# Kernel tuning notes

Measured on AMD Instinct MI355X. Metric: run time of the kernel, lower is better.

The kernel has to match this reference:

```python
import jax, jax.numpy as jnp
import numpy as np

K = 7          # kernel_size (window)
PAD = (K - 1) // 2  # SAME padding for stride 1


def setup_inputs() -> dict:
    key = jax.random.key(0)
    ks = jax.random.split(key, 7)
    B, H, W, C, F = 8, 128, 128, 256, 256
    rs = F // 2  # rel_size
    return {
        "x": jax.random.normal(ks[0], (B, H, W, C), jnp.float32),
        "Wq": jax.random.normal(ks[1], (C, F), jnp.float32) * 0.05,
        "Wk": jax.random.normal(ks[2], (C, F), jnp.float32) * 0.05,
        "Wv": jax.random.normal(ks[3], (C, F), jnp.float32) * 0.05,
        "rel_x": jax.random.normal(ks[4], (rs, K), jnp.float32) * 0.05,
        "rel_y": jax.random.normal(ks[5], (F - rs, K), jnp.float32) * 0.05,
        "bias": jax.random.normal(ks[6], (1, 1, 1, F), jnp.float32) * (1.0 / np.sqrt(F).astype(np.float32)),
    }


def reference(x, Wq, Wk, Wv, rel_x, rel_y, bias):
    B, H, W, C = x.shape
    rs = rel_x.shape[0]
    # 1x1 conv projections (single group)
    q = jnp.einsum('bhwc,cf->bhwf', x, Wq)
    k = jnp.einsum('bhwc,cf->bhwf', x, Wk)
    v = jnp.einsum('bhwc,cf->bhwf', x, Wv)
    kp = jnp.pad(k, ((0, 0), (PAD, PAD), (PAD, PAD), (0, 0)))
    vp = jnp.pad(v, ((0, 0), (PAD, PAD), (PAD, PAD), (0, 0)))
    # window scores: sum_c q * shifted(k) -> [b,h,w,kh,kw]; avoids im2col blowup
    scores = jnp.stack([
        jnp.stack([jnp.einsum('bhwf,bhwf->bhw', q, kp[:, i:i + H, j:j + W, :])
                   for j in range(K)], axis=-1)
        for i in range(K)], axis=-2)
    # relative position terms: x-half broadcasts along rows (kh), y-half along cols (kw)
    qx = jnp.einsum('bhwx,xk->bhwk', q[..., :rs], rel_x)
    qy = jnp.einsum('bhwy,yk->bhwk', q[..., rs:], rel_y)
    scores = scores + qx[:, :, :, None, :] + qy[:, :, :, :, None]
    attn = jax.nn.softmax(scores.reshape(B, H, W, K * K), axis=-1).reshape(B, H, W, K, K)
    # attention-weighted sum over the window for each channel
    out = sum(attn[:, :, :, i, j][..., None] * vp[:, i:i + H, j:j + W, :]
              for i in range(K) for j in range(K))
    return out + bias
```

## Files before the change

### kernel.cpp

```cpp
#include <hip/hip_runtime.h>
#include <hip/hip_fp16.h>
#include <stdint.h>

typedef _Float16 half8 __attribute__((ext_vector_type(8)));
typedef _Float16 half2v __attribute__((ext_vector_type(2)));
typedef __attribute__((ext_vector_type(4))) float f32x4;

__device__ __forceinline__ unsigned short f2h(float f) {
  __half h = __float2half(f);
  unsigned short u; __builtin_memcpy(&u, &h, 2); return u;
}
__device__ __forceinline__ unsigned pk2h(float a, float b) {
  auto v = __builtin_amdgcn_cvt_pkrtz(a, b);
  unsigned u; __builtin_memcpy(&u, &v, 4); return u;
}
__device__ __forceinline__ half2v h2cast(unsigned u) {
  half2v v; __builtin_memcpy(&v, &u, 4); return v;
}

#if __has_builtin(__builtin_amdgcn_fdot2)
__device__ __forceinline__ float dot2(half2v a, half2v b, float c) {
  return __builtin_amdgcn_fdot2(a, b, c, false);
}
#else
__device__ __forceinline__ float dot2(half2v a, half2v b, float c) {
  return c + (float)a[0] * (float)b[0] + (float)a[1] * (float)b[1];
}
#endif

__device__ __forceinline__ void gl_lds16(const void* g, void* l) {
  __builtin_amdgcn_global_load_lds(
      (const __attribute__((address_space(1))) void*)g,
      (__attribute__((address_space(3))) void*)l, 16, 0, 0);
}

__global__ __launch_bounds__(256) void prep(const float* __restrict__ x,
                                            const float* __restrict__ Wq,
                                            const float* __restrict__ Wk,
                                            const float* __restrict__ Wv,
                                            unsigned short* __restrict__ xh,
                                            unsigned short* __restrict__ Wb) {
  const int bid = blockIdx.x;
  if (bid < 16384) {
    const size_t i = ((size_t)bid * 256 + threadIdx.x) * 8;
    float4 a = *(const float4*)&x[i];
    float4 b = *(const float4*)&x[i + 4];
    uint4 o;
    o.x = pk2h(a.x, a.y); o.y = pk2h(a.z, a.w);
    o.z = pk2h(b.x, b.y); o.w = pk2h(b.z, b.w);
    *(uint4*)&xh[i] = o;
  } else {
    const int e = bid - 16384;
    const int w = e >> 8;
    const int n = e & 255;
    const float* W = (w == 0) ? Wq : ((w == 1) ? Wk : Wv);
    const int k = threadIdx.x;
    Wb[(size_t)e * 256 + k] = f2h(W[(size_t)k * 256 + n]);
  }
}

__global__ __launch_bounds__(256) void qkv_gemm(const unsigned short* __restrict__ xh,
                                                const unsigned short* __restrict__ Wb,
                                                unsigned short* __restrict__ qkv) {
  __shared__ unsigned char ldsb[32768];

  const int tid = threadIdx.x;
  const int l = tid & 63, l15 = l & 15, l4 = l >> 4;
  const int wv = tid >> 6, wr = wv >> 1, wc = wv & 1;

  const int pid = blockIdx.x;
  const int cid = (pid & 7) * 768 + (pid >> 3);
  const int by = cid / 6;
  const int bx = cid - by * 6;
  const size_t row0 = (size_t)by * 128;
  const int n0 = bx * 128;

  const int rbase0 = wv * 32, rbase1 = wv * 32 + 16;
  const int rA0 = rbase0 + (l >> 2), rA1 = rbase1 + (l >> 2);
  const int q0 = (l & 3) ^ ((rA0 >> 1) & 3), q1 = (l & 3) ^ ((rA1 >> 1) & 3);
  const unsigned short* gA0 = xh + (row0 + rA0) * 256 + q0 * 8;
  const unsigned short* gA1 = xh + (row0 + rA1) * 256 + q1 * 8;
  const unsigned short* gB0 = Wb + (size_t)(n0 + rA0) * 256 + q0 * 8;
  const unsigned short* gB1 = Wb + (size_t)(n0 + rA1) * 256 + q1 * 8;

  f32x4 acc[4][4] = {};

  auto stage = [&](int s, int d) {
    gl_lds16(gA0 + s * 32, &ldsb[d * 8192 + rbase0 * 64]);
    gl_lds16(gA1 + s * 32, &ldsb[d * 8192 + rbase1 * 64]);
    gl_lds16(gB0 + s * 32, &ldsb[16384 + d * 8192 + rbase0 * 64]);
    gl_lds16(gB1 + s * 32, &ldsb[16384 + d * 8192 + rbase1 * 64]);
  };

  stage(0, 0);
  __syncthreads();

  for (int s = 0; s < 8; ++s) {
    const int d = s & 1;
    if (s < 7) stage(s + 1, d ^ 1);
    half8 af[4], bf[4];
#pragma unroll
    for (int m = 0; m < 4; ++m) {
      const int r = wr * 64 + m * 16 + l15;
      af[m] = *(const half8*)&ldsb[d * 8192 + r * 64 + ((l4 ^ ((r >> 1) & 3)) * 16)];
    }
#pragma unroll
    for (int n = 0; n < 4; ++n) {
      const int r = wc * 64 + n * 16 + l15;
      bf[n] = *(const half8*)&ldsb[16384 + d * 8192 + r * 64 + ((l4 ^ ((r >> 1) & 3)) * 16)];
    }
#pragma unroll
    for (int n = 0; n < 4; ++n)
#pragma unroll
      for (int m = 0; m < 4; ++m)
        acc[m][n] = __builtin_amdgcn_mfma_f32_16x16x32_f16(af[m], bf[n], acc[m][n], 0, 0, 0);
    __syncthreads();
  }

#pragma unroll
  for (int m = 0; m < 4; ++m)
#pragma unroll
    for (int n = 0; n < 4; ++n) {
      const int ng = n0 + wc * 64 + n * 16 + l15;
      unsigned short* op = qkv + (size_t)(ng >> 8) * 33554432 + (ng & 255);
#pragma unroll
      for (int r = 0; r < 4; ++r) {
        const size_t grow = row0 + wr * 64 + m * 16 + l4 * 4 + r;
        op[grow * 256] = f2h(acc[m][n][r]);
      }
    }
}

__global__ __launch_bounds__(256) void qrel(const unsigned short* __restrict__ q,
                                            const float* __restrict__ relx,
                                            const float* __restrict__ rely,
                                            unsigned short* __restrict__ qr) {
  __shared__ unsigned wpk[896];
  for (int i = threadIdx.x; i < 896; i += 256) {
    const int hf = (i >= 448) ? 1 : 0;
    const int r = i - hf * 448;
    const int c2 = r / 7, j = r - c2 * 7;
    const float* R = hf ? rely : relx;
    wpk[i] = pk2h(R[(2 * c2) * 7 + j], R[(2 * c2 + 1) * 7 + j]);
  }
  __syncthreads();
  const size_t pix = (size_t)blockIdx.x * 256 + threadIdx.x;
  const uint4* qp = (const uint4*)(q + pix * 256);
  float ax[7] = {0, 0, 0, 0, 0, 0, 0}, ay[7] = {0, 0, 0, 0, 0, 0, 0};
#pragma unroll
  for (int g = 0; g < 32; ++g) {
    const uint4 u = qp[g];
    const int c2b = (g & 15) * 4;
    if (g < 16) {
#pragma unroll
      for (int j = 0; j < 7; ++j) {
        float s = ax[j];
        s = dot2(h2cast(u.x), h2cast(wpk[(c2b + 0) * 7 + j]), s);
        s = dot2(h2cast(u.y), h2cast(wpk[(c2b + 1) * 7 + j]), s);
        s = dot2(h2cast(u.z), h2cast(wpk[(c2b + 2) * 7 + j]), s);
        s = dot2(h2cast(u.w), h2cast(wpk[(c2b + 3) * 7 + j]), s);
        ax[j] = s;
      }
    } else {
#pragma unroll
      for (int j = 0; j < 7; ++j) {
        float s = ay[j];
        s = dot2(h2cast(u.x), h2cast(wpk[448 + (c2b + 0) * 7 + j]), s);
        s = dot2(h2cast(u.y), h2cast(wpk[448 + (c2b + 1) * 7 + j]), s);
        s = dot2(h2cast(u.z), h2cast(wpk[448 + (c2b + 2) * 7 + j]), s);
        s = dot2(h2cast(u.w), h2cast(wpk[448 + (c2b + 3) * 7 + j]), s);
        ay[j] = s;
      }
    }
  }
  uint4 o0, o1;
  o0.x = pk2h(ax[0], ax[1]); o0.y = pk2h(ax[2], ax[3]);
  o0.z = pk2h(ax[4], ax[5]); o0.w = pk2h(ax[6], ay[0]);
  o1.x = pk2h(ay[1], ay[2]); o1.y = pk2h(ay[3], ay[4]);
  o1.z = pk2h(ay[5], ay[6]); o1.w = 0;
  uint4* dst = (uint4*)(qr + pix * 512);
  dst[0] = o0; dst[1] = o1;
}

__global__ __launch_bounds__(512, 2) void attn(const unsigned short* __restrict__ qkv,
                                               const float* __restrict__ bias,
                                               const unsigned short* __restrict__ qrelb,
                                               float* __restrict__ out) {
  __shared__ unsigned short kv[2][4][4256];

  const int tid = threadIdx.x;
  const int wv = tid >> 6;
  const int lo = tid & 15, hi = (tid >> 4) & 3;
  const int rp = wv >> 1;
  const int ch16 = (wv & 1) * 16;

  const int q = tid >> 7;
  const int pa = (tid >> 5) & 3;
  const int pc = tid & 31;

  const int pid = blockIdx.x;
  const int cid = (pid & 7) * 64 + (pid >> 3);
  const int ht = cid & 15, wt = (cid >> 4) & 3, b = cid >> 6;

  const int hA = ht * 8 + 2 * pa, wA = wt * 32 + pc;
  const size_t pixA = (size_t)((b * 128 + hA) * 128 + wA);
  const size_t pixB = pixA + 128;
  const int pxA = 2 * pa * 32 + pc;
  const int pxB = pxA + 32;

  const unsigned short* qb = qkv;
  const unsigned short* kb = qkv + 33554432;
  const unsigned short* vb = qkv + 67108864;

  const int pr0 = tid / 38, pc0 = tid - pr0 * 38;
  const int gh0 = ht * 8 + pr0 - 3, gw0 = wt * 32 + pc0 - 3;
  const bool ok0 = ((unsigned)gh0 < 128u) && ((unsigned)gw0 < 128u);
  const long long go0 = ((long long)((b * 128 + gh0) * 128 + gw0)) * 256;

  const int p1 = tid + 512;
  const int pr1 = p1 / 38, pc1 = p1 - pr1 * 38;
  const int gh1 = ht * 8 + pr1 - 3, gw1 = wt * 32 + pc1 - 3;
  const bool ok1 = (p1 < 532) && ((unsigned)gh1 < 128u) && ((unsigned)gw1 < 128u);
  const long long go1 = ((long long)((b * 128 + gh1) * 128 + gw1)) * 256;

  auto stage = [&](const unsigned short* base, int c, int d) {
#pragma unroll
    for (int g = 0; g < 4; ++g) {
      if (ok0) gl_lds16(base + go0 + c * 32 + g * 8, &kv[d][g][wv * 512]);
      if (ok1) gl_lds16(base + go1 + c * 32 + g * 8, &kv[d][g][4096]);
    }
  };

  auto zero_oob = [&]() {
    const uint4 z = make_uint4(0u, 0u, 0u, 0u);
    for (int p = tid; p < 532; p += 512) {
      const int pr = p / 38, pcx = p - pr * 38;
      const int gh = ht * 8 + pr - 3, gw = wt * 32 + pcx - 3;
      if (!((unsigned)gh < 128u && (unsigned)gw < 128u)) {
#pragma unroll
        for (int d = 0; d < 2; ++d)
#pragma unroll
          for (int g = 0; g < 4; ++g)
            *(uint4*)&kv[d][g][p * 8] = z;
      }
    }
  };

  zero_oob();
  stage(kb, 0, 0);
  __syncthreads();

  int slot0[7];
#pragma unroll
  for (int t = 0; t < 7; ++t) {
    const int p = t * 16 + lo;
    const int ur = p / 14, uc = p - ur * 14;
    slot0[t] = (2 * rp + ur) * 38 + ch16 + uc;
  }
  const size_t qpix =
      (size_t)((b * 128 + ht * 8 + 2 * rp + (lo >> 3)) * 128 + wt * 32 + ch16 + (lo & 7));
  const unsigned short* qlane = qb + qpix * 256 + hi * 8;

  f32x4 acc[2][7] = {};

  for (int s = 0; s < 8; ++s) {
    const int d = s & 1;
    if (s < 7) stage(kb, s + 1, d ^ 1);
    half8 qf[2];
#pragma unroll
    for (int g = 0; g < 2; ++g)
      qf[g] = *(const half8*)(qlane + (size_t)g * 2048 + s * 32);
    const unsigned short* kpl = &kv[d][hi][0];
    __builtin_amdgcn_s_setprio(1);
    half8 kf[7][2];
#pragma unroll
    for (int t = 0; t < 7; ++t) {
      const unsigned short* kt = kpl + slot0[t] * 8;
      kf[t][0] = *(const half8*)(kt);
      kf[t][1] = *(const half8*)(kt + 64);
    }
#pragma unroll
    for (int t = 0; t < 7; ++t) {
      acc[0][t] = __builtin_amdgcn_mfma_f32_16x16x32_f16(qf[0], kf[t][0], acc[0][t], 0, 0, 0);
      acc[1][t] = __builtin_amdgcn_mfma_f32_16x16x32_f16(qf[1], kf[t][1], acc[1][t], 0, 0, 0);
    }
    __builtin_amdgcn_s_setprio(0);
    __syncthreads();
  }

  float* pbuf = (float*)&kv[0][0][0];
#pragma unroll
  for (int t = 0; t < 7; ++t) {
    const int p = t * 16 + lo;
    const int ur = p / 14, uc = p - ur * 14;
#pragma unroll
    for (int r = 0; r < 4; ++r) {
      const int qq = hi * 4 + r;
      const int di = ur - (qq >> 3), dj = uc - (qq & 7);
      if (((unsigned)di < 7u) && ((unsigned)dj < 7u)) {
        const int pslot = di * 7 + dj;
#pragma unroll
        for (int g = 0; g < 2; ++g) {
          const int prow_ = (2 * rp + (qq >> 3)) * 32 + ch16 + 8 * g + (qq & 7);
          pbuf[prow_ * 52 + pslot] = acc[g][t][r];
        }
      }
    }
  }
  __syncthreads();

  unsigned pwp[49];
  {
    float sc[49];
    const float* prow = pbuf + pxA * 52;
#pragma unroll
    for (int k = 0; k < 12; ++k) {
      const float4 v = ((const float4*)prow)[k];
      sc[k * 4 + 0] = v.x; sc[k * 4 + 1] = v.y;
      sc[k * 4 + 2] = v.z; sc[k * 4 + 3] = v.w;
    }
    sc[48] = prow[48];
    const uint4* rpq = (const uint4*)(qrelb + pixA * 512);
    uint4 r0 = rpq[0], r1 = rpq[1];
    half2v a0 = h2cast(r0.x), a1 = h2cast(r0.y), a2 = h2cast(r0.z), a3 = h2cast(r0.w);
    half2v b0 = h2cast(r1.x), b1 = h2cast(r1.y), b2 = h2cast(r1.z);
    float qx[7] = {a0[0], a0[1], a1[0], a1[1], a2[0], a2[1], a3[0]};
    float qy[7] = {a3[1], b0[0], b0[1], b1[0], b1[1], b2[0], b2[1]};
#pragma unroll
    for (int i = 0; i < 7; ++i)
#pragma unroll
      for (int j = 0; j < 7; ++j) sc[i * 7 + j] += qx[j] + qy[i];
    float mx = sc[0];
#pragma unroll
    for (int t = 1; t < 49; ++t) mx = fmaxf(mx, sc[t]);
    float sum = 0.0f;
#pragma unroll
    for (int t = 0; t < 49; ++t) {
      float e = __expf(sc[t] - mx);
      sc[t] = e;
      sum += e;
    }
    const float invs = 1.0f / sum;
#pragma unroll
    for (int t = 0; t < 49; ++t) pwp[t] = (unsigned)f2h(sc[t] * invs);
  }
  {
    float sc[49];
    const float* prow = pbuf + pxB * 52;
#pragma unroll
    for (int k = 0; k < 12; ++k) {
      const float4 v = ((const float4*)prow)[k];
      sc[k * 4 + 0] = v.x; sc[k * 4 + 1] = v.y;
      sc[k * 4 + 2] = v.z; sc[k * 4 + 3] = v.w;
    }
    sc[48] = prow[48];
    const uint4* rpq = (const uint4*)(qrelb + pixB * 512);
    uint4 r0 = rpq[0], r1 = rpq[1];
    half2v a0 = h2cast(r0.x), a1 = h2cast(r0.y), a2 = h2cast(r0.z), a3 = h2cast(r0.w);
    half2v b0 = h2cast(r1.x), b1 = h2cast(r1.y), b2 = h2cast(r1.z);
    float qx[7] = {a0[0], a0[1], a1[0], a1[1], a2[0], a2[1], a3[0]};
    float qy[7] = {a3[1], b0[0], b0[1], b1[0], b1[1], b2[0], b2[1]};
#pragma unroll
    for (int i = 0; i < 7; ++i)
#pragma unroll
      for (int j = 0; j < 7; ++j) sc[i * 7 + j] += qx[j] + qy[i];
    float mx = sc[0];
#pragma unroll
    for (int t = 1; t < 49; ++t) mx = fmaxf(mx, sc[t]);
    float sum = 0.0f;
#pragma unroll
    for (int t = 0; t < 49; ++t) {
      float e = __expf(sc[t] - mx);
      sc[t] = e;
      sum += e;
    }
    const float invs = 1.0f / sum;
#pragma unroll
    for (int t = 0; t < 49; ++t) pwp[t] |= ((unsigned)f2h(sc[t] * invs)) << 16;
  }
  __syncthreads();

  zero_oob();
  stage(vb, 0, 0);
  __syncthreads();

  for (int s = 0; s < 8; ++s) {
    const int d = s & 1;
    const int f0 = s * 32 + q * 8;
    if (s < 7) stage(vb, s + 1, d ^ 1);
    half2v accA[4], accB[4];
#pragma unroll
    for (int a2 = 0; a2 < 4; ++a2) {
      accA[a2] = half2v{(_Float16)0, (_Float16)0};
      accB[a2] = half2v{(_Float16)0, (_Float16)0};
    }
    __builtin_amdgcn_s_setprio(1);
#pragma unroll
    for (int ub = 0; ub < 4; ++ub) {
      const int u0 = 2 * ub, u1 = u0 + 1;
      const int r0b = ((2 * pa + u0) * 38 + pc) * 8;
      const int r1b = ((2 * pa + u1) * 38 + pc) * 8;
      uint4 ua[14];
#pragma unroll
      for (int j = 0; j < 7; ++j) {
        ua[j] = *(const uint4*)&kv[d][q][r0b + j * 8];
        ua[7 + j] = *(const uint4*)&kv[d][q][r1b + j * 8];
      }
#pragma unroll
      for (int j = 0; j < 7; ++j) {
        {
          const half2v pp = h2cast(pwp[u0 * 7 + j]);
          const half2v p2 = half2v{pp[0], pp[0]};
          accA[0] += p2 * h2cast(ua[j].x);
          accA[1] += p2 * h2cast(ua[j].y);
          accA[2] += p2 * h2cast(ua[j].z);
          accA[3] += p2 * h2cast(ua[j].w);
        }
        if (ub > 0) {
          const half2v pp = h2cast(pwp[(u0 - 1) * 7 + j]);
          const half2v p2 = half2v{pp[1], pp[1]};
          accB[0] += p2 * h2cast(ua[j].x);
          accB[1] += p2 * h2cast(ua[j].y);
          accB[2] += p2 * h2cast(ua[j].z);
          accB[3] += p2 * h2cast(ua[j].w);
        }
      }
#pragma unroll
      for (int j = 0; j < 7; ++j) {
        if (ub < 3) {
          const half2v pp = h2cast(pwp[u1 * 7 + j]);
          const half2v p2 = half2v{pp[0], pp[0]};
          accA[0] += p2 * h2cast(ua[7 + j].x);
          accA[1] += p2 * h2cast(ua[7 + j].y);
          accA[2] += p2 * h2cast(ua[7 + j].z);
          accA[3] += p2 * h2cast(ua[7 + j].w);
        }
        {
          const half2v pp = h2cast(pwp[(u1 - 1) * 7 + j]);
          const half2v p2 = half2v{pp[1], pp[1]};
          accB[0] += p2 * h2cast(ua[7 + j].x);
          accB[1] += p2 * h2cast(ua[7 + j].y);
          accB[2] += p2 * h2cast(ua[7 + j].z);
          accB[3] += p2 * h2cast(ua[7 + j].w);
        }
      }
    }
    __builtin_amdgcn_s_setprio(0);
#pragma unroll
    for (int fq = 0; fq < 2; ++fq) {
      float4 bv = *(const float4*)&bias[f0 + fq * 4];
      float4 oA, oB;
      oA.x = (float)accA[fq * 2 + 0][0] + bv.x;
      oA.y = (float)accA[fq * 2 + 0][1] + bv.y;
      oA.z = (float)accA[fq * 2 + 1][0] + bv.z;
      oA.w = (float)accA[fq * 2 + 1][1] + bv.w;
      oB.x = (float)accB[fq * 2 + 0][0] + bv.x;
      oB.y = (float)accB[fq * 2 + 0][1] + bv.y;
      oB.z = (float)accB[fq * 2 + 1][0] + bv.z;
      oB.w = (float)accB[fq * 2 + 1][1] + bv.w;
      *(float4*)&out[pixA * 256 + f0 + fq * 4] = oA;
      *(float4*)&out[pixB * 256 + f0 + fq * 4] = oB;
    }
    if (s < 7) __syncthreads();
  }
}

extern "C" void kernel_launch(void* const* d_in, const int* in_sizes, int n_in,
                              void* d_out, int out_size, void* d_ws, size_t ws_size,
                              hipStream_t stream) {
  const float* x = (const float*)d_in[0];
  const float* Wq = (const float*)d_in[1];
  const float* Wk = (const float*)d_in[2];
  const float* Wv = (const float*)d_in[3];
  const float* relx = (const float*)d_in[4];
  const float* rely = (const float*)d_in[5];
  const float* bias = (const float*)d_in[6];
  float* out = (float*)d_out;

  unsigned short* xh = (unsigned short*)d_out;
  unsigned short* qrl = (unsigned short*)d_out;
  unsigned short* Wb = (unsigned short*)d_ws;
  unsigned short* qkv = (unsigned short*)((char*)d_ws + 393216);

  prep<<<dim3(17152), dim3(256), 0, stream>>>(x, Wq, Wk, Wv, xh, Wb);
  qkv_gemm<<<dim3(6144), dim3(256), 0, stream>>>(xh, Wb, qkv);
  qrel<<<dim3(512), dim3(256), 0, stream>>>(qkv, relx, rely, qrl);
  attn<<<dim3(512), dim3(512), 0, stream>>>(qkv, bias, qrl, out);
}
```

Measured before the change: 273.7 us.

## Fuse relative-position projection into attention kernel using already-loaded q fragments

Removes the separate qrel kernel and computes the q·rel_x / q·rel_y terms inside the attention kernel. It reuses the q fragments already loaded for the score MFMAs, does dot2 accumulation per stage, reduces across lanes with shuffles, and stores packed results in LDS for the softmax. This drops a kernel launch and a global round-trip of the q tensor plus the qrel buffer. In exchange it adds LDS usage, extra VALU work and register pressure in the main loop, which could lower occupancy.

```diff
diff --git a/kernel.cpp b/kernel.cpp
--- a/kernel.cpp
+++ b/kernel.cpp
@@ -131,62 +131,14 @@
     }
 }
 
-__global__ __launch_bounds__(256) void qrel(const unsigned short* __restrict__ q,
-                                            const float* __restrict__ relx,
-                                            const float* __restrict__ rely,
-                                            unsigned short* __restrict__ qr) {
-  __shared__ unsigned wpk[896];
-  for (int i = threadIdx.x; i < 896; i += 256) {
-    const int hf = (i >= 448) ? 1 : 0;
-    const int r = i - hf * 448;
-    const int c2 = r / 7, j = r - c2 * 7;
-    const float* R = hf ? rely : relx;
-    wpk[i] = pk2h(R[(2 * c2) * 7 + j], R[(2 * c2 + 1) * 7 + j]);
-  }
-  __syncthreads();
-  const size_t pix = (size_t)blockIdx.x * 256 + threadIdx.x;
-  const uint4* qp = (const uint4*)(q + pix * 256);
-  float ax[7] = {0, 0, 0, 0, 0, 0, 0}, ay[7] = {0, 0, 0, 0, 0, 0, 0};
-#pragma unroll
-  for (int g = 0; g < 32; ++g) {
-    const uint4 u = qp[g];
-    const int c2b = (g & 15) * 4;
-    if (g < 16) {
-#pragma unroll
-      for (int j = 0; j < 7; ++j) {
-        float s = ax[j];
-        s = dot2(h2cast(u.x), h2cast(wpk[(c2b + 0) * 7 + j]), s);
-        s = dot2(h2cast(u.y), h2cast(wpk[(c2b + 1) * 7 + j]), s);
-        s = dot2(h2cast(u.z), h2cast(wpk[(c2b + 2) * 7 + j]), s);
-        s = dot2(h2cast(u.w), h2cast(wpk[(c2b + 3) * 7 + j]), s);
-        ax[j] = s;
-      }
-    } else {
-#pragma unroll
-      for (int j = 0; j < 7; ++j) {
-        float s = ay[j];
-        s = dot2(h2cast(u.x), h2cast(wpk[448 + (c2b + 0) * 7 + j]), s);
-        s = dot2(h2cast(u.y), h2cast(wpk[448 + (c2b + 1) * 7 + j]), s);
-        s = dot2(h2cast(u.z), h2cast(wpk[448 + (c2b + 2) * 7 + j]), s);
-        s = dot2(h2cast(u.w), h2cast(wpk[448 + (c2b + 3) * 7 + j]), s);
-        ay[j] = s;
-      }
-    }
-  }
-  uint4 o0, o1;
-  o0.x = pk2h(ax[0], ax[1]); o0.y = pk2h(ax[2], ax[3]);
-  o0.z = pk2h(ax[4], ax[5]); o0.w = pk2h(ax[6], ay[0]);
-  o1.x = pk2h(ay[1], ay[2]); o1.y = pk2h(ay[3], ay[4]);
-  o1.z = pk2h(ay[5], ay[6]); o1.w = 0;
-  uint4* dst = (uint4*)(qr + pix * 512);
-  dst[0] = o0; dst[1] = o1;
-}
-
 __global__ __launch_bounds__(512, 2) void attn(const unsigned short* __restrict__ qkv,
                                                const float* __restrict__ bias,
-                                               const unsigned short* __restrict__ qrelb,
+                                               const float* __restrict__ relx,
+                                               const float* __restrict__ rely,
                                                float* __restrict__ out) {
   __shared__ unsigned short kv[2][4][4256];
+  __shared__ unsigned wpk[896];
+  __shared__ unsigned qrl_lds[256 * 7];
 
   const int tid = threadIdx.x;
   const int wv = tid >> 6;
@@ -246,6 +198,14 @@
     }
   };
 
+  for (int i = tid; i < 896; i += 512) {
+    const int hf = (i >= 448) ? 1 : 0;
+    const int r = i - hf * 448;
+    const int c2 = r / 7, j = r - c2 * 7;
+    const float* R = hf ? rely : relx;
+    wpk[i] = pk2h(R[(2 * c2) * 7 + j], R[(2 * c2 + 1) * 7 + j]);
+  }
+
   zero_oob();
   stage(kb, 0, 0);
   __syncthreads();
@@ -262,6 +222,7 @@
   const unsigned short* qlane = qb + qpix * 256 + hi * 8;
 
   f32x4 acc[2][7] = {};
+  float qxp[2][7] = {}, qyp[2][7] = {};
 
   for (int s = 0; s < 8; ++s) {
     const int d = s & 1;
@@ -285,7 +246,66 @@
       acc[1][t] = __builtin_amdgcn_mfma_f32_16x16x32_f16(qf[1], kf[t][1], acc[1][t], 0, 0, 0);
     }
     __builtin_amdgcn_s_setprio(0);
+    if (s < 4) {
+      const int cb = s * 16 + hi * 4;
+#pragma unroll
+      for (int g = 0; g < 2; ++g) {
+        uint4 qw; __builtin_memcpy(&qw, &qf[g], 16);
+#pragma unroll
+        for (int j = 0; j < 7; ++j) {
+          float v = qxp[g][j];
+          v = dot2(h2cast(qw.x), h2cast(wpk[(cb + 0) * 7 + j]), v);
+          v = dot2(h2cast(qw.y), h2cast(wpk[(cb + 1) * 7 + j]), v);
+          v = dot2(h2cast(qw.z), h2cast(wpk[(cb + 2) * 7 + j]), v);
+          v = dot2(h2cast(qw.w), h2cast(wpk[(cb + 3) * 7 + j]), v);
+          qxp[g][j] = v;
+        }
+      }
+    } else {
+      const int cb = (s - 4) * 16 + hi * 4;
+#pragma unroll
+      for (int g = 0; g < 2; ++g) {
+        uint4 qw; __builtin_memcpy(&qw, &qf[g], 16);
+#pragma unroll
+        for (int j = 0; j < 7; ++j) {
+          float v = qyp[g][j];
+          v = dot2(h2cast(qw.x), h2cast(wpk[448 + (cb + 0) * 7 + j]), v);
+          v = dot2(h2cast(qw.y), h2cast(wpk[448 + (cb + 1) * 7 + j]), v);
+          v = dot2(h2cast(qw.z), h2cast(wpk[448 + (cb + 2) * 7 + j]), v);
+          v = dot2(h2cast(qw.w), h2cast(wpk[448 + (cb + 3) * 7 + j]), v);
+          qyp[g][j] = v;
+        }
+      }
+    }
     __syncthreads();
+  }
+
+#pragma unroll
+  for (int g = 0; g < 2; ++g)
+#pragma unroll
+    for (int j = 0; j < 7; ++j) {
+      float vx = qxp[g][j];
+      vx += __shfl_xor(vx, 16, 64);
+      vx += __shfl_xor(vx, 32, 64);
+      qxp[g][j] = vx;
+      float vy = qyp[g][j];
+      vy += __shfl_xor(vy, 16, 64);
+      vy += __shfl_xor(vy, 32, 64);
+      qyp[g][j] = vy;
+    }
+  if (hi == 0) {
+#pragma unroll
+    for (int g = 0; g < 2; ++g) {
+      const int prow_ = (2 * rp + (lo >> 3)) * 32 + ch16 + 8 * g + (lo & 7);
+      unsigned* dst = &qrl_lds[prow_ * 7];
+      dst[0] = pk2h(qxp[g][0], qxp[g][1]);
+      dst[1] = pk2h(qxp[g][2], qxp[g][3]);
+      dst[2] = pk2h(qxp[g][4], qxp[g][5]);
+      dst[3] = pk2h(qxp[g][6], qyp[g][0]);
+      dst[4] = pk2h(qyp[g][1], qyp[g][2]);
+      dst[5] = pk2h(qyp[g][3], qyp[g][4]);
+      dst[6] = pk2h(qyp[g][5], qyp[g][6]);
+    }
   }
 
   float* pbuf = (float*)&kv[0][0][0];
@@ -320,10 +340,9 @@
       sc[k * 4 + 2] = v.z; sc[k * 4 + 3] = v.w;
     }
     sc[48] = prow[48];
-    const uint4* rpq = (const uint4*)(qrelb + pixA * 512);
-    uint4 r0 = rpq[0], r1 = rpq[1];
-    half2v a0 = h2cast(r0.x), a1 = h2cast(r0.y), a2 = h2cast(r0.z), a3 = h2cast(r0.w);
-    half2v b0 = h2cast(r1.x), b1 = h2cast(r1.y), b2 = h2cast(r1.z);
+    const unsigned* qr = &qrl_lds[pxA * 7];
+    half2v a0 = h2cast(qr[0]), a1 = h2cast(qr[1]), a2 = h2cast(qr[2]), a3 = h2cast(qr[3]);
+    half2v b0 = h2cast(qr[4]), b1 = h2cast(qr[5]), b2 = h2cast(qr[6]);
     float qx[7] = {a0[0], a0[1], a1[0], a1[1], a2[0], a2[1], a3[0]};
     float qy[7] = {a3[1], b0[0], b0[1], b1[0], b1[1], b2[0], b2[1]};
 #pragma unroll
@@ -354,10 +373,9 @@
       sc[k * 4 + 2] = v.z; sc[k * 4 + 3] = v.w;
     }
     sc[48] = prow[48];
-    const uint4* rpq = (const uint4*)(qrelb + pixB * 512);
-    uint4 r0 = rpq[0], r1 = rpq[1];
-    half2v a0 = h2cast(r0.x), a1 = h2cast(r0.y), a2 = h2cast(r0.z), a3 = h2cast(r0.w);
-    half2v b0 = h2cast(r1.x), b1 = h2cast(r1.y), b2 = h2cast(r1.z);
+    const unsigned* qr = &qrl_lds[pxB * 7];
+    half2v a0 = h2cast(qr[0]), a1 = h2cast(qr[1]), a2 = h2cast(qr[2]), a3 = h2cast(qr[3]);
+    half2v b0 = h2cast(qr[4]), b1 = h2cast(qr[5]), b2 = h2cast(qr[6]);
     float qx[7] = {a0[0], a0[1], a1[0], a1[1], a2[0], a2[1], a3[0]};
     float qy[7] = {a3[1], b0[0], b0[1], b1[0], b1[1], b2[0], b2[1]};
 #pragma unroll
@@ -478,12 +496,10 @@
   float* out = (float*)d_out;
 
   unsigned short* xh = (unsigned short*)d_out;
-  unsigned short* qrl = (unsigned short*)d_out;
   unsigned short* Wb = (unsigned short*)d_ws;
   unsigned short* qkv = (unsigned short*)((char*)d_ws + 393216);
 
   prep<<<dim3(17152), dim3(256), 0, stream>>>(x, Wq, Wk, Wv, xh, Wb);
   qkv_gemm<<<dim3(6144), dim3(256), 0, stream>>>(xh, Wb, qkv);
-  qrel<<<dim3(512), dim3(256), 0, stream>>>(qkv, relx, rely, qrl);
-  attn<<<dim3(512), dim3(512), 0, stream>>>(qkv, bias, qrl, out);
-}
+  attn<<<dim3(512), dim3(512), 0, stream>>>(qkv, bias, relx, rely, out);
+}
```

New measurement: 276.8 us. No clear change (+1.1%).
